# Performance work log

Measured on AMD Instinct MI355X. Metric: run time of the kernel, lower is better.

The kernel has to match this reference:

```python
import jax, jax.numpy as jnp
import numpy as np

N_NODES = 50000


def sage_conv(x, src, dst, Wl, bl, Wr):
    # PyG SAGEConv (aggr='mean'): out = lin_l(mean_{j in N(i)} x_j) + lin_r(x_i)
    # lin_l has bias, lin_r (root) has no bias.
    n = x.shape[0]
    agg = jax.ops.segment_sum(x[src], dst, num_segments=n)          # [N, d_in]
    cnt = jax.ops.segment_sum(jnp.ones((src.shape[0],), x.dtype), dst, num_segments=n)
    mean = agg / jnp.maximum(cnt, 1.0)[:, None]
    return mean @ Wl + bl + x @ Wr


def setup_inputs() -> dict:
    key = jax.random.key(0)
    k1, k2, k3, k4, k5, k6, k7 = jax.random.split(key, 7)
    in_c, hid_c, out_c = 128, 128, 2
    x = jax.random.normal(k1, (N_NODES, in_c), dtype=jnp.float32)
    edge_index = jax.random.randint(k2, (2, 800000), 0, N_NODES, dtype=jnp.int64)
    s1 = 1.0 / np.sqrt(in_c)
    s2 = 1.0 / np.sqrt(hid_c)
    return {
        "x": x,
        "edge_index": edge_index,
        "W1l": jax.random.uniform(k3, (in_c, hid_c), jnp.float32, -s1, s1),
        "b1l": jnp.zeros((hid_c,), jnp.float32),
        "W1r": jax.random.uniform(k4, (in_c, hid_c), jnp.float32, -s1, s1),
        "W2l": jax.random.uniform(k5, (hid_c, out_c), jnp.float32, -s2, s2),
        "b2l": jnp.zeros((out_c,), jnp.float32),
        "W2r": jax.random.uniform(k6, (hid_c, out_c), jnp.float32, -s2, s2),
    }


def reference(x, edge_index, W1l, b1l, W1r, W2l, b2l, W2r):
    src, dst = edge_index[0], edge_index[1]
    h = jax.nn.relu(sage_conv(x, src, dst, W1l, b1l, W1r))
    return sage_conv(h, src, dst, W2l, b2l, W2r)
```

## Files before the change

kernel.cpp:

```cpp
#include <hip/hip_runtime.h>

#define N_NODES 50000
#define N_PAD 50176
#define N_EDGES 800000
#define C 128
#define NB 784
#define NPB 64
#define CBCAP 1408
#define B1_BUCK 391
#define TOBF_B 6250
#define ZPAD_B 11
#define PACK_B 16
#define SG_T 512

typedef unsigned short ushort_t;
typedef unsigned int uint_t;
typedef __attribute__((ext_vector_type(8))) short bf16x8;
typedef __attribute__((ext_vector_type(4))) float f32x4;

__device__ __forceinline__ uint_t f2bf(float f) {
    uint_t u = __float_as_uint(f);
    u += 0x7fffu + ((u >> 16) & 1u);
    return u >> 16;
}
__device__ __forceinline__ float bflo(uint_t u) { return __uint_as_float(u << 16); }
__device__ __forceinline__ float bfhi(uint_t u) { return __uint_as_float(u & 0xffff0000u); }

__global__ __launch_bounds__(256) void bucket1_kernel(
    const int* __restrict__ src, const int* __restrict__ dst,
    int* __restrict__ gcur, uint_t* __restrict__ cb,
    const float* __restrict__ x, ushort_t* __restrict__ xh,
    const float* __restrict__ W1l, const float* __restrict__ W1r,
    ushort_t* __restrict__ Bp) {
    int b = blockIdx.x;
    int t = threadIdx.x;
    if (b < B1_BUCK) {
        __shared__ int hist[NB];
        __shared__ int offs[NB];
        for (int i = t; i < NB; i += 256) hist[i] = 0;
        __syncthreads();
        int tid = b * 256 + t;
        bool act = tid < N_EDGES / 8;
        int4 s0, s1, d0, d1;
        if (act) {
            s0 = ((const int4*)src)[2 * tid];
            s1 = ((const int4*)src)[2 * tid + 1];
            d0 = ((const int4*)dst)[2 * tid];
            d1 = ((const int4*)dst)[2 * tid + 1];
            atomicAdd(&hist[d0.x >> 6], 1);
            atomicAdd(&hist[d0.y >> 6], 1);
            atomicAdd(&hist[d0.z >> 6], 1);
            atomicAdd(&hist[d0.w >> 6], 1);
            atomicAdd(&hist[d1.x >> 6], 1);
            atomicAdd(&hist[d1.y >> 6], 1);
            atomicAdd(&hist[d1.z >> 6], 1);
            atomicAdd(&hist[d1.w >> 6], 1);
        }
        __syncthreads();
        for (int i = t; i < NB; i += 256) {
            offs[i] = atomicAdd(&gcur[i], hist[i]);
            hist[i] = 0;
        }
        __syncthreads();
        if (act) {
            int ss[8] = {s0.x, s0.y, s0.z, s0.w, s1.x, s1.y, s1.z, s1.w};
            int dd[8] = {d0.x, d0.y, d0.z, d0.w, d1.x, d1.y, d1.z, d1.w};
            #pragma unroll
            for (int i = 0; i < 8; i++) {
                int bkt = dd[i] >> 6;
                int pos = offs[bkt] + atomicAdd(&hist[bkt], 1);
                if (pos < CBCAP)
                    cb[(size_t)bkt * CBCAP + pos] = ((uint_t)ss[i] << 16) | (uint_t)dd[i];
            }
        }
    } else if (b < B1_BUCK + TOBF_B) {
        int i = (b - B1_BUCK) * 256 + t;
        float4 v = ((const float4*)x)[i];
        uint_t lo = f2bf(v.x) | (f2bf(v.y) << 16);
        uint_t hi = f2bf(v.z) | (f2bf(v.w) << 16);
        ((uint2*)xh)[i] = make_uint2(lo, hi);
    } else if (b < B1_BUCK + TOBF_B + ZPAD_B) {
        int i = (b - B1_BUCK - TOBF_B) * 256 + t;
        if (i < (N_PAD - N_NODES) * C / 8)
            ((uint4*)(xh + (size_t)N_NODES * C))[i] = make_uint4(0, 0, 0, 0);
    } else {
        int p = (b - B1_BUCK - TOBF_B - ZPAD_B) * 256 + t;
        int lane = p & 63;
        int pair = p >> 6;
        int kk = pair & 7;
        int nt = pair >> 3;
        int n = lane & 15, quad = lane >> 4;
        int col = nt * 16 + n;
        int k0 = kk * 32 + quad * 8;
        uint_t w[4];
        #pragma unroll
        for (int jj = 0; jj < 4; jj++) {
            int ka = k0 + 2 * jj, kb = k0 + 2 * jj + 1;
            float fa = (ka < C) ? W1l[ka * C + col] : W1r[(ka - C) * C + col];
            float fb = (kb < C) ? W1l[kb * C + col] : W1r[(kb - C) * C + col];
            w[jj] = f2bf(fa) | (f2bf(fb) << 16);
        }
        ((uint4*)(Bp + (size_t)p * 8))[0] = make_uint4(w[0], w[1], w[2], w[3]);
    }
}

__device__ __forceinline__ void bf8_acc(float* a, const uint4 v) {
    a[0] += bflo(v.x); a[1] += bfhi(v.x);
    a[2] += bflo(v.y); a[3] += bfhi(v.y);
    a[4] += bflo(v.z); a[5] += bfhi(v.z);
    a[6] += bflo(v.w); a[7] += bfhi(v.w);
}

__global__ __launch_bounds__(SG_T) void sortgather_kernel(
    const int* __restrict__ gcur, const uint_t* __restrict__ cb,
    const ushort_t* __restrict__ xh, ushort_t* __restrict__ esorted,
    int* __restrict__ nodeoff, int* __restrict__ cursor,
    ushort_t* __restrict__ msb) {
    __shared__ uint_t srun[CBCAP];
    __shared__ ushort_t sidx[CBCAP];
    __shared__ int cnt[NPB], offs[NPB], cur[NPB];
    int b = blockIdx.x, t = threadIdx.x;
    if (t < NPB) { cnt[t] = 0; cur[t] = 0; }
    __syncthreads();

    int len = gcur[b];
    if (len > CBCAP) len = CBCAP;
    const uint_t* run = cb + (size_t)b * CBCAP;
    for (int e = t; e < len; e += SG_T) {
        uint_t rec = run[e];
        srun[e] = rec;
        atomicAdd(&cnt[rec & (NPB - 1)], 1);
    }
    __syncthreads();

    if (t < 64) {
        int v = cnt[t];
        int s = v;
        #pragma unroll
        for (int o = 1; o < 64; o <<= 1) {
            int u = __shfl_up(s, o, 64);
            if (t >= o) s += u;
        }
        offs[t] = s - v;
    }
    __syncthreads();

    for (int e = t; e < len; e += SG_T) {
        uint_t rec = srun[e];
        int local = rec & (NPB - 1);
        int pos = offs[local] + atomicAdd(&cur[local], 1);
        sidx[pos] = (ushort_t)(rec >> 16);
    }
    __syncthreads();

    for (int e = t; 2 * e < len; e += SG_T) {
        uint_t v = (uint_t)sidx[2 * e];
        if (2 * e + 1 < len) v |= (uint_t)sidx[2 * e + 1] << 16;
        ((uint_t*)esorted)[(size_t)b * (CBCAP / 2) + e] = v;
    }
    if (t < NPB) {
        int g = b * NPB + t;
        nodeoff[g] = b * CBCAP + offs[t];
        cursor[g] = cnt[t];
    }

    int grp = t >> 4, q = t & 15;
    #pragma unroll
    for (int rep = 0; rep < 2; rep++) {
        int local = grp + rep * 32;
        int d = cnt[local];
        int start = offs[local];
        float a[8] = {0,0,0,0,0,0,0,0};
        float c[8] = {0,0,0,0,0,0,0,0};
        int e = 0;
        for (; e + 8 <= d; e += 8) {
            int s0 = sidx[start + e + 0], s1 = sidx[start + e + 1];
            int s2 = sidx[start + e + 2], s3 = sidx[start + e + 3];
            int s4 = sidx[start + e + 4], s5 = sidx[start + e + 5];
            int s6 = sidx[start + e + 6], s7 = sidx[start + e + 7];
            uint4 v0 = ((const uint4*)(xh + (size_t)s0 * C))[q];
            uint4 v1 = ((const uint4*)(xh + (size_t)s1 * C))[q];
            uint4 v2 = ((const uint4*)(xh + (size_t)s2 * C))[q];
            uint4 v3 = ((const uint4*)(xh + (size_t)s3 * C))[q];
            uint4 v4 = ((const uint4*)(xh + (size_t)s4 * C))[q];
            uint4 v5 = ((const uint4*)(xh + (size_t)s5 * C))[q];
            uint4 v6 = ((const uint4*)(xh + (size_t)s6 * C))[q];
            uint4 v7 = ((const uint4*)(xh + (size_t)s7 * C))[q];
            bf8_acc(a, v0); bf8_acc(c, v1); bf8_acc(a, v2); bf8_acc(c, v3);
            bf8_acc(a, v4); bf8_acc(c, v5); bf8_acc(a, v6); bf8_acc(c, v7);
        }
        for (; e + 4 <= d; e += 4) {
            int s0 = sidx[start + e + 0], s1 = sidx[start + e + 1];
            int s2 = sidx[start + e + 2], s3 = sidx[start + e + 3];
            uint4 v0 = ((const uint4*)(xh + (size_t)s0 * C))[q];
            uint4 v1 = ((const uint4*)(xh + (size_t)s1 * C))[q];
            uint4 v2 = ((const uint4*)(xh + (size_t)s2 * C))[q];
            uint4 v3 = ((const uint4*)(xh + (size_t)s3 * C))[q];
            bf8_acc(a, v0); bf8_acc(c, v1); bf8_acc(a, v2); bf8_acc(c, v3);
        }
        for (; e < d; e++) {
            uint4 v = ((const uint4*)(xh + (size_t)sidx[start + e] * C))[q];
            bf8_acc(a, v);
        }
        float inv = 1.0f / fmaxf((float)d, 1.0f);
        uint4 o;
        o.x = f2bf((a[0] + c[0]) * inv) | (f2bf((a[1] + c[1]) * inv) << 16);
        o.y = f2bf((a[2] + c[2]) * inv) | (f2bf((a[3] + c[3]) * inv) << 16);
        o.z = f2bf((a[4] + c[4]) * inv) | (f2bf((a[5] + c[5]) * inv) << 16);
        o.w = f2bf((a[6] + c[6]) * inv) | (f2bf((a[7] + c[7]) * inv) << 16);
        ((uint4*)(msb + (size_t)(b * NPB + local) * C))[q] = o;
    }
}

__global__ __launch_bounds__(512) void gemm_mfma(
    const ushort_t* __restrict__ msb, const ushort_t* __restrict__ xh,
    const ushort_t* __restrict__ Bp, const float* __restrict__ b1l,
    const float* __restrict__ W2l, const float* __restrict__ W2r,
    const float* __restrict__ b2l, float* __restrict__ z, float* __restrict__ out) {
    __shared__ ushort_t sB[2 * C * C];
    int t = threadIdx.x;
    #pragma unroll
    for (int i = 0; i < 8; i++)
        ((uint4*)sB)[i * 512 + t] = ((const uint4*)Bp)[i * 512 + t];
    __syncthreads();

    int wid = t >> 6, lane = t & 63;
    int m = lane & 15, quad = lane >> 4;
    int base = blockIdx.x * 128 + wid * 16;

    const ushort_t* a_ms = msb + (size_t)(base + m) * C + quad * 8;
    const ushort_t* a_xh = xh  + (size_t)(base + m) * C + quad * 8;
    bf16x8 aw[8];
    #pragma unroll
    for (int kk = 0; kk < 4; kk++) aw[kk]     = *(const bf16x8*)(a_ms + kk * 32);
    #pragma unroll
    for (int kk = 0; kk < 4; kk++) aw[4 + kk] = *(const bf16x8*)(a_xh + kk * 32);

    f32x4 acc[8];
    #pragma unroll
    for (int nt = 0; nt < 8; nt++) acc[nt] = (f32x4){0.f, 0.f, 0.f, 0.f};

    const bf16x8* bp = (const bf16x8*)sB;
    #pragma unroll
    for (int kk = 0; kk < 8; kk++) {
        bf16x8 a = aw[kk];
        #pragma unroll
        for (int nt = 0; nt < 8; nt++) {
            bf16x8 bfr = bp[(nt * 8 + kk) * 64 + lane];
            acc[nt] = __builtin_amdgcn_mfma_f32_16x16x32_bf16(a, bfr, acc[nt], 0, 0, 0);
        }
    }

    float zz0[4] = {0,0,0,0}, zz1[4] = {0,0,0,0};
    float rr0[4] = {0,0,0,0}, rr1[4] = {0,0,0,0};
    #pragma unroll
    for (int nt = 0; nt < 8; nt++) {
        int col = nt * 16 + m;
        float bias = b1l[col];
        float2 wl = ((const float2*)W2l)[col];
        float2 wr = ((const float2*)W2r)[col];
        #pragma unroll
        for (int reg = 0; reg < 4; reg++) {
            float h = fmaxf(acc[nt][reg] + bias, 0.0f);
            zz0[reg] = fmaf(h, wl.x, zz0[reg]);
            zz1[reg] = fmaf(h, wl.y, zz1[reg]);
            rr0[reg] = fmaf(h, wr.x, rr0[reg]);
            rr1[reg] = fmaf(h, wr.y, rr1[reg]);
        }
    }
    float bl0 = b2l[0], bl1 = b2l[1];
    #pragma unroll
    for (int reg = 0; reg < 4; reg++) {
        float a0 = zz0[reg], a1 = zz1[reg], c0 = rr0[reg], c1 = rr1[reg];
        #pragma unroll
        for (int off = 8; off > 0; off >>= 1) {
            a0 += __shfl_down(a0, off, 16);
            a1 += __shfl_down(a1, off, 16);
            c0 += __shfl_down(c0, off, 16);
            c1 += __shfl_down(c1, off, 16);
        }
        if (m == 0) {
            int node = base + quad * 4 + reg;
            if (node < N_NODES) {
                z[node * 2 + 0]   = a0;
                z[node * 2 + 1]   = a1;
                out[node * 2 + 0] = c0 + bl0;
                out[node * 2 + 1] = c1 + bl1;
            }
        }
    }
}

__global__ __launch_bounds__(256) void final_kernel(
    const float* __restrict__ z, const int* __restrict__ nodeoff,
    const int* __restrict__ cursor, const ushort_t* __restrict__ esorted,
    float* __restrict__ out) {
    int t = threadIdx.x;
    int sub = t & 15;
    int node = blockIdx.x * 16 + (t >> 4);
    int d = cursor[node];
    const ushort_t* lst = esorted + nodeoff[node];
    float a0 = 0.0f, a1 = 0.0f;
    for (int e = sub; e < d; e += 16) {
        float2 v = ((const float2*)z)[lst[e]];
        a0 += v.x; a1 += v.y;
    }
    #pragma unroll
    for (int off = 8; off > 0; off >>= 1) {
        a0 += __shfl_down(a0, off);
        a1 += __shfl_down(a1, off);
    }
    if (sub == 0) {
        float inv = 1.0f / fmaxf((float)d, 1.0f);
        out[node * 2 + 0] += a0 * inv;
        out[node * 2 + 1] += a1 * inv;
    }
}

extern "C" void kernel_launch(void* const* d_in, const int* in_sizes, int n_in,
                              void* d_out, int out_size, void* d_ws, size_t ws_size,
                              hipStream_t stream) {
    const float* x   = (const float*)d_in[0];
    const int*   ei  = (const int*)d_in[1];
    const float* W1l = (const float*)d_in[2];
    const float* b1l = (const float*)d_in[3];
    const float* W1r = (const float*)d_in[4];
    const float* W2l = (const float*)d_in[5];
    const float* b2l = (const float*)d_in[6];
    const float* W2r = (const float*)d_in[7];
    float* out = (float*)d_out;

    const int* src = ei;
    const int* dst = ei + N_EDGES;

    int* gcur        = (int*)d_ws;
    uint_t* cb       = (uint_t*)(gcur + 1024);
    ushort_t* esorted = (ushort_t*)(cb + (size_t)NB * CBCAP);
    int* nodeoff     = (int*)(esorted + (size_t)NB * CBCAP);
    int* cursor      = nodeoff + N_PAD;
    ushort_t* xh     = (ushort_t*)(cursor + N_PAD);
    ushort_t* msb    = xh + (size_t)N_PAD * C;
    ushort_t* Bp     = msb + (size_t)N_PAD * C;
    float* z         = (float*)(Bp + 2 * C * C);

    hipMemsetAsync(gcur, 0, NB * sizeof(int), stream);

    bucket1_kernel<<<B1_BUCK + TOBF_B + ZPAD_B + PACK_B, 256, 0, stream>>>(
        src, dst, gcur, cb, x, xh, W1l, W1r, Bp);
    sortgather_kernel<<<NB, SG_T, 0, stream>>>(gcur, cb, xh, esorted, nodeoff, cursor, msb);
    gemm_mfma<<<392, 512, 0, stream>>>(msb, xh, Bp, b1l, W2l, W2r, b2l, z, out);
    final_kernel<<<N_NODES / 16, 256, 0, stream>>>(z, nodeoff, cursor, esorted, out);
}
```

Baseline: 153.5 us.

## Split sort and gather kernels; store bf16 features in channel-sliced planes

Stores the bf16 copy of x as four 32-channel planes, so each gather pass touches a smaller, cache-resident slice. The fused sort+gather kernel is split into a sort kernel and a separate gather_slice kernel. In gather_slice, block index bits pick the plane so neighbouring blocks share a slice. The GEMM reads its root operand from the planes. The aim is better L2 hit rates for the random neighbour reads, at the cost of an extra launch and re-reading the edge lists four times.

```diff
diff --git a/kernel.cpp b/kernel.cpp
--- a/kernel.cpp
+++ b/kernel.cpp
@@ -11,7 +11,8 @@
 #define TOBF_B 6250
 #define ZPAD_B 11
 #define PACK_B 16
-#define SG_T 512
+#define PLANE_U ((size_t)N_PAD * 32)
+#define GS_B 6272
 
 typedef unsigned short ushort_t;
 typedef unsigned int uint_t;
@@ -78,11 +79,18 @@
         float4 v = ((const float4*)x)[i];
         uint_t lo = f2bf(v.x) | (f2bf(v.y) << 16);
         uint_t hi = f2bf(v.z) | (f2bf(v.w) << 16);
-        ((uint2*)xh)[i] = make_uint2(lo, hi);
+        int node = i >> 5, c = i & 31;
+        int plane = c >> 3, part = c & 7;
+        ((uint2*)(xh + (size_t)plane * PLANE_U + node * 32 + part * 4))[0] =
+            make_uint2(lo, hi);
     } else if (b < B1_BUCK + TOBF_B + ZPAD_B) {
         int i = (b - B1_BUCK - TOBF_B) * 256 + t;
-        if (i < (N_PAD - N_NODES) * C / 8)
-            ((uint4*)(xh + (size_t)N_NODES * C))[i] = make_uint4(0, 0, 0, 0);
+        if (i < 2816) {
+            int plane = i / 704, rem = i % 704;
+            int node = N_NODES + (rem >> 2), part = rem & 3;
+            ((uint4*)(xh + (size_t)plane * PLANE_U + node * 32 + part * 8))[0] =
+                make_uint4(0, 0, 0, 0);
+        }
     } else {
         int p = (b - B1_BUCK - TOBF_B - ZPAD_B) * 256 + t;
         int lane = p & 63;
@@ -104,6 +112,59 @@
     }
 }
 
+__global__ __launch_bounds__(256) void sort_kernel(
+    const int* __restrict__ gcur, const uint_t* __restrict__ cb,
+    ushort_t* __restrict__ esorted, int* __restrict__ nodeoff,
+    int* __restrict__ cursor) {
+    __shared__ uint_t srun[CBCAP];
+    __shared__ ushort_t sidx[CBCAP];
+    __shared__ int cnt[NPB], offs[NPB], cur[NPB];
+    int b = blockIdx.x, t = threadIdx.x;
+    if (t < NPB) { cnt[t] = 0; cur[t] = 0; }
+    __syncthreads();
+
+    int len = gcur[b];
+    if (len > CBCAP) len = CBCAP;
+    const uint_t* run = cb + (size_t)b * CBCAP;
+    for (int e = t; e < len; e += 256) {
+        uint_t rec = run[e];
+        srun[e] = rec;
+        atomicAdd(&cnt[rec & (NPB - 1)], 1);
+    }
+    __syncthreads();
+
+    if (t < 64) {
+        int v = cnt[t];
+        int s = v;
+        #pragma unroll
+        for (int o = 1; o < 64; o <<= 1) {
+            int u = __shfl_up(s, o, 64);
+            if (t >= o) s += u;
+        }
+        offs[t] = s - v;
+    }
+    __syncthreads();
+
+    for (int e = t; e < len; e += 256) {
+        uint_t rec = srun[e];
+        int local = rec & (NPB - 1);
+        int pos = offs[local] + atomicAdd(&cur[local], 1);
+        sidx[pos] = (ushort_t)(rec >> 16);
+    }
+    __syncthreads();
+
+    for (int e = t; 2 * e < len; e += 256) {
+        uint_t v = (uint_t)sidx[2 * e];
+        if (2 * e + 1 < len) v |= (uint_t)sidx[2 * e + 1] << 16;
+        ((uint_t*)esorted)[(size_t)b * (CBCAP / 2) + e] = v;
+    }
+    if (t < NPB) {
+        int g = b * NPB + t;
+        nodeoff[g] = b * CBCAP + offs[t];
+        cursor[g] = cnt[t];
+    }
+}
+
 __device__ __forceinline__ void bf8_acc(float* a, const uint4 v) {
     a[0] += bflo(v.x); a[1] += bfhi(v.x);
     a[2] += bflo(v.y); a[3] += bfhi(v.y);
@@ -111,105 +172,55 @@
     a[6] += bflo(v.w); a[7] += bfhi(v.w);
 }
 
-__global__ __launch_bounds__(SG_T) void sortgather_kernel(
-    const int* __restrict__ gcur, const uint_t* __restrict__ cb,
-    const ushort_t* __restrict__ xh, ushort_t* __restrict__ esorted,
-    int* __restrict__ nodeoff, int* __restrict__ cursor,
+__global__ __launch_bounds__(128) void gather_slice(
+    const ushort_t* __restrict__ xh, const ushort_t* __restrict__ esorted,
+    const int* __restrict__ nodeoff, const int* __restrict__ cursor,
     ushort_t* __restrict__ msb) {
-    __shared__ uint_t srun[CBCAP];
-    __shared__ ushort_t sidx[CBCAP];
-    __shared__ int cnt[NPB], offs[NPB], cur[NPB];
     int b = blockIdx.x, t = threadIdx.x;
-    if (t < NPB) { cnt[t] = 0; cur[t] = 0; }
-    __syncthreads();
-
-    int len = gcur[b];
-    if (len > CBCAP) len = CBCAP;
-    const uint_t* run = cb + (size_t)b * CBCAP;
-    for (int e = t; e < len; e += SG_T) {
-        uint_t rec = run[e];
-        srun[e] = rec;
-        atomicAdd(&cnt[rec & (NPB - 1)], 1);
-    }
-    __syncthreads();
-
-    if (t < 64) {
-        int v = cnt[t];
-        int s = v;
-        #pragma unroll
-        for (int o = 1; o < 64; o <<= 1) {
-            int u = __shfl_up(s, o, 64);
-            if (t >= o) s += u;
-        }
-        offs[t] = s - v;
-    }
-    __syncthreads();
-
-    for (int e = t; e < len; e += SG_T) {
-        uint_t rec = srun[e];
-        int local = rec & (NPB - 1);
-        int pos = offs[local] + atomicAdd(&cur[local], 1);
-        sidx[pos] = (ushort_t)(rec >> 16);
-    }
-    __syncthreads();
-
-    for (int e = t; 2 * e < len; e += SG_T) {
-        uint_t v = (uint_t)sidx[2 * e];
-        if (2 * e + 1 < len) v |= (uint_t)sidx[2 * e + 1] << 16;
-        ((uint_t*)esorted)[(size_t)b * (CBCAP / 2) + e] = v;
-    }
-    if (t < NPB) {
-        int g = b * NPB + t;
-        nodeoff[g] = b * CBCAP + offs[t];
-        cursor[g] = cnt[t];
-    }
-
-    int grp = t >> 4, q = t & 15;
-    #pragma unroll
-    for (int rep = 0; rep < 2; rep++) {
-        int local = grp + rep * 32;
-        int d = cnt[local];
-        int start = offs[local];
-        float a[8] = {0,0,0,0,0,0,0,0};
-        float c[8] = {0,0,0,0,0,0,0,0};
-        int e = 0;
-        for (; e + 8 <= d; e += 8) {
-            int s0 = sidx[start + e + 0], s1 = sidx[start + e + 1];
-            int s2 = sidx[start + e + 2], s3 = sidx[start + e + 3];
-            int s4 = sidx[start + e + 4], s5 = sidx[start + e + 5];
-            int s6 = sidx[start + e + 6], s7 = sidx[start + e + 7];
-            uint4 v0 = ((const uint4*)(xh + (size_t)s0 * C))[q];
-            uint4 v1 = ((const uint4*)(xh + (size_t)s1 * C))[q];
-            uint4 v2 = ((const uint4*)(xh + (size_t)s2 * C))[q];
-            uint4 v3 = ((const uint4*)(xh + (size_t)s3 * C))[q];
-            uint4 v4 = ((const uint4*)(xh + (size_t)s4 * C))[q];
-            uint4 v5 = ((const uint4*)(xh + (size_t)s5 * C))[q];
-            uint4 v6 = ((const uint4*)(xh + (size_t)s6 * C))[q];
-            uint4 v7 = ((const uint4*)(xh + (size_t)s7 * C))[q];
-            bf8_acc(a, v0); bf8_acc(c, v1); bf8_acc(a, v2); bf8_acc(c, v3);
-            bf8_acc(a, v4); bf8_acc(c, v5); bf8_acc(a, v6); bf8_acc(c, v7);
-        }
-        for (; e + 4 <= d; e += 4) {
-            int s0 = sidx[start + e + 0], s1 = sidx[start + e + 1];
-            int s2 = sidx[start + e + 2], s3 = sidx[start + e + 3];
-            uint4 v0 = ((const uint4*)(xh + (size_t)s0 * C))[q];
-            uint4 v1 = ((const uint4*)(xh + (size_t)s1 * C))[q];
-            uint4 v2 = ((const uint4*)(xh + (size_t)s2 * C))[q];
-            uint4 v3 = ((const uint4*)(xh + (size_t)s3 * C))[q];
-            bf8_acc(a, v0); bf8_acc(c, v1); bf8_acc(a, v2); bf8_acc(c, v3);
-        }
-        for (; e < d; e++) {
-            uint4 v = ((const uint4*)(xh + (size_t)sidx[start + e] * C))[q];
-            bf8_acc(a, v);
-        }
-        float inv = 1.0f / fmaxf((float)d, 1.0f);
-        uint4 o;
-        o.x = f2bf((a[0] + c[0]) * inv) | (f2bf((a[1] + c[1]) * inv) << 16);
-        o.y = f2bf((a[2] + c[2]) * inv) | (f2bf((a[3] + c[3]) * inv) << 16);
-        o.z = f2bf((a[4] + c[4]) * inv) | (f2bf((a[5] + c[5]) * inv) << 16);
-        o.w = f2bf((a[6] + c[6]) * inv) | (f2bf((a[7] + c[7]) * inv) << 16);
-        ((uint4*)(msb + (size_t)(b * NPB + local) * C))[q] = o;
-    }
+    int slice = (b & 7) >> 1;
+    int chunk = (b >> 3) * 2 + (b & 1);
+    int g = t >> 2, lane = t & 3;
+    int node = chunk * 32 + g;
+    int d = cursor[node];
+    const ushort_t* lst = esorted + nodeoff[node];
+    const ushort_t* plane = xh + (size_t)slice * PLANE_U + lane * 8;
+
+    float a[8] = {0,0,0,0,0,0,0,0};
+    float c8[8] = {0,0,0,0,0,0,0,0};
+    int e = 0;
+    for (; e + 8 <= d; e += 8) {
+        int s0 = lst[e + 0], s1 = lst[e + 1], s2 = lst[e + 2], s3 = lst[e + 3];
+        int s4 = lst[e + 4], s5 = lst[e + 5], s6 = lst[e + 6], s7 = lst[e + 7];
+        uint4 v0 = *(const uint4*)(plane + (size_t)s0 * 32);
+        uint4 v1 = *(const uint4*)(plane + (size_t)s1 * 32);
+        uint4 v2 = *(const uint4*)(plane + (size_t)s2 * 32);
+        uint4 v3 = *(const uint4*)(plane + (size_t)s3 * 32);
+        uint4 v4 = *(const uint4*)(plane + (size_t)s4 * 32);
+        uint4 v5 = *(const uint4*)(plane + (size_t)s5 * 32);
+        uint4 v6 = *(const uint4*)(plane + (size_t)s6 * 32);
+        uint4 v7 = *(const uint4*)(plane + (size_t)s7 * 32);
+        bf8_acc(a, v0); bf8_acc(c8, v1); bf8_acc(a, v2); bf8_acc(c8, v3);
+        bf8_acc(a, v4); bf8_acc(c8, v5); bf8_acc(a, v6); bf8_acc(c8, v7);
+    }
+    for (; e + 4 <= d; e += 4) {
+        int s0 = lst[e + 0], s1 = lst[e + 1], s2 = lst[e + 2], s3 = lst[e + 3];
+        uint4 v0 = *(const uint4*)(plane + (size_t)s0 * 32);
+        uint4 v1 = *(const uint4*)(plane + (size_t)s1 * 32);
+        uint4 v2 = *(const uint4*)(plane + (size_t)s2 * 32);
+        uint4 v3 = *(const uint4*)(plane + (size_t)s3 * 32);
+        bf8_acc(a, v0); bf8_acc(c8, v1); bf8_acc(a, v2); bf8_acc(c8, v3);
+    }
+    for (; e < d; e++) {
+        uint4 v = *(const uint4*)(plane + (size_t)lst[e] * 32);
+        bf8_acc(a, v);
+    }
+    float inv = 1.0f / fmaxf((float)d, 1.0f);
+    uint4 o;
+    o.x = f2bf((a[0] + c8[0]) * inv) | (f2bf((a[1] + c8[1]) * inv) << 16);
+    o.y = f2bf((a[2] + c8[2]) * inv) | (f2bf((a[3] + c8[3]) * inv) << 16);
+    o.z = f2bf((a[4] + c8[4]) * inv) | (f2bf((a[5] + c8[5]) * inv) << 16);
+    o.w = f2bf((a[6] + c8[6]) * inv) | (f2bf((a[7] + c8[7]) * inv) << 16);
+    ((uint4*)(msb + (size_t)node * C + slice * 32 + lane * 8))[0] = o;
 }
 
 __global__ __launch_bounds__(512) void gemm_mfma(
@@ -227,14 +238,15 @@
     int wid = t >> 6, lane = t & 63;
     int m = lane & 15, quad = lane >> 4;
     int base = blockIdx.x * 128 + wid * 16;
-
-    const ushort_t* a_ms = msb + (size_t)(base + m) * C + quad * 8;
-    const ushort_t* a_xh = xh  + (size_t)(base + m) * C + quad * 8;
+    int node = base + m;
+
+    const ushort_t* a_ms = msb + (size_t)node * C + quad * 8;
     bf16x8 aw[8];
     #pragma unroll
-    for (int kk = 0; kk < 4; kk++) aw[kk]     = *(const bf16x8*)(a_ms + kk * 32);
-    #pragma unroll
-    for (int kk = 0; kk < 4; kk++) aw[4 + kk] = *(const bf16x8*)(a_xh + kk * 32);
+    for (int kk = 0; kk < 4; kk++) aw[kk] = *(const bf16x8*)(a_ms + kk * 32);
+    #pragma unroll
+    for (int kk = 0; kk < 4; kk++)
+        aw[4 + kk] = *(const bf16x8*)(xh + (size_t)kk * PLANE_U + node * 32 + quad * 8);
 
     f32x4 acc[8];
     #pragma unroll
@@ -280,12 +292,12 @@
             c1 += __shfl_down(c1, off, 16);
         }
         if (m == 0) {
-            int node = base + quad * 4 + reg;
-            if (node < N_NODES) {
-                z[node * 2 + 0]   = a0;
-                z[node * 2 + 1]   = a1;
-                out[node * 2 + 0] = c0 + bl0;
-                out[node * 2 + 1] = c1 + bl1;
+            int onode = base + quad * 4 + reg;
+            if (onode < N_NODES) {
+                z[onode * 2 + 0]   = a0;
+                z[onode * 2 + 1]   = a1;
+                out[onode * 2 + 0] = c0 + bl0;
+                out[onode * 2 + 1] = c1 + bl1;
             }
         }
     }
@@ -333,21 +345,22 @@
     const int* src = ei;
     const int* dst = ei + N_EDGES;
 
-    int* gcur        = (int*)d_ws;
-    uint_t* cb       = (uint_t*)(gcur + 1024);
+    int* gcur         = (int*)d_ws;
+    uint_t* cb        = (uint_t*)(gcur + 1024);
     ushort_t* esorted = (ushort_t*)(cb + (size_t)NB * CBCAP);
-    int* nodeoff     = (int*)(esorted + (size_t)NB * CBCAP);
-    int* cursor      = nodeoff + N_PAD;
-    ushort_t* xh     = (ushort_t*)(cursor + N_PAD);
-    ushort_t* msb    = xh + (size_t)N_PAD * C;
-    ushort_t* Bp     = msb + (size_t)N_PAD * C;
-    float* z         = (float*)(Bp + 2 * C * C);
+    int* nodeoff      = (int*)(esorted + (size_t)NB * CBCAP);
+    int* cursor       = nodeoff + N_PAD;
+    ushort_t* xh      = (ushort_t*)(cursor + N_PAD);
+    ushort_t* msb     = xh + 4 * PLANE_U;
+    ushort_t* Bp      = msb + (size_t)N_PAD * C;
+    float* z          = (float*)(Bp + 2 * C * C);
 
     hipMemsetAsync(gcur, 0, NB * sizeof(int), stream);
 
     bucket1_kernel<<<B1_BUCK + TOBF_B + ZPAD_B + PACK_B, 256, 0, stream>>>(
         src, dst, gcur, cb, x, xh, W1l, W1r, Bp);
-    sortgather_kernel<<<NB, SG_T, 0, stream>>>(gcur, cb, xh, esorted, nodeoff, cursor, msb);
+    sort_kernel<<<NB, 256, 0, stream>>>(gcur, cb, esorted, nodeoff, cursor);
+    gather_slice<<<GS_B, 128, 0, stream>>>(xh, esorted, nodeoff, cursor, msb);
     gemm_mfma<<<392, 512, 0, stream>>>(msb, xh, Bp, b1l, W2l, W2r, b2l, z, out);
     final_kernel<<<N_NODES / 16, 256, 0, stream>>>(z, nodeoff, cursor, esorted, out);
 }
```

Result: faster. 149.9 us (-2.3%).
